# Kernel optimization log

Measured on AMD Instinct MI355X. Metric: run time of the kernel, lower is better.

## Reference

```python
import jax, jax.numpy as jnp
import numpy as np

N = 50000          # nodes
E = 1600000        # edges (avg degree 32)
IN_C, HID_C, OUT_C = 256, 256, 256


def setup_inputs() -> dict:
    key = jax.random.key(0)
    ks = jax.random.split(key, 10)
    x = jax.random.normal(ks[0], (N, IN_C), dtype=jnp.float32)
    edge_index = jax.random.randint(ks[1], (2, E), 0, N, dtype=jnp.int32)
    edge_weight = jax.random.uniform(ks[2], (E,), dtype=jnp.float32)
    W1 = jax.random.normal(ks[3], (IN_C, HID_C), dtype=jnp.float32) / np.float32(np.sqrt(IN_C))
    b1 = jnp.zeros((HID_C,), dtype=jnp.float32)
    W2 = jax.random.normal(ks[4], (HID_C, OUT_C), dtype=jnp.float32) / np.float32(np.sqrt(HID_C))
    b2 = jnp.zeros((OUT_C,), dtype=jnp.float32)
    Wf = jax.random.normal(ks[5], (OUT_C, 1), dtype=jnp.float32) / np.float32(np.sqrt(OUT_C))
    bf = jnp.zeros((1,), dtype=jnp.float32)
    return {"x": x, "edge_index": edge_index, "edge_weight": edge_weight,
            "W1": W1, "b1": b1, "W2": W2, "b2": b2, "Wf": Wf, "bf": bf}


def _gcn_norm(edge_index, edge_weight, num_nodes, dtype):
    # add self loops with weight 1 (PyG gcn_norm default, add_self_loops=True)
    src, dst = edge_index[0], edge_index[1]
    loop = jnp.arange(num_nodes, dtype=edge_index.dtype)
    src_f = jnp.concatenate([src, loop])
    dst_f = jnpp_concat = jnp.concatenate([dst, loop])
    w_f = jnp.concatenate([edge_weight.astype(dtype), jnp.ones((num_nodes,), dtype)])
    # degree over destination nodes (flow source_to_target)
    deg = jax.ops.segment_sum(w_f, dst_f, num_segments=num_nodes)
    dinv = jnp.where(deg > 0, jax.lax.rsqrt(deg), jnp.array(0.0, dtype))
    norm = dinv[src_f] * w_f * dinv[dst_f]   # [E + N]
    return src_f, dst_f, norm


def _gcn_conv(x, src_f, dst_f, norm, W, b):
    h = x @ W                                    # transform first: [N, out]
    msg = h[src_f] * norm[:, None]               # gather + edge-wise scale: [E+N, out]
    agg = jax.ops.segment_sum(msg, dst_f, num_segments=x.shape[0])  # scatter-add
    return agg + b


def reference(x, edge_index, edge_weight, W1, b1, W2, b2, Wf, bf):
    n = x.shape[0]
    src_f, dst_f, norm = _gcn_norm(edge_index, edge_weight, n, x.dtype)
    h = jax.nn.relu(_gcn_conv(x, src_f, dst_f, norm, W1, b1))
    h = jax.nn.relu(_gcn_conv(h, src_f, dst_f, norm, W2, b2))
    out = h @ Wf + bf
    return out
```

## Files before the change

kernel.cpp:

```cpp
#include <hip/hip_runtime.h>
#include <hip/hip_bf16.h>
#include <cstdint>

#define IN_C 256

typedef __attribute__((ext_vector_type(8))) short bf16x8;
typedef __attribute__((ext_vector_type(8))) short s16x8;
typedef __attribute__((ext_vector_type(4))) short s16x4;
typedef __attribute__((ext_vector_type(8))) unsigned short u16x8;
typedef __attribute__((ext_vector_type(4))) float f32x4;

#define FIXED_SCALE 33554432.0f
#define FIXED_INV   (1.0f / 33554432.0f)
#define DEG_MASK    ((1ULL << 40) - 1)

__device__ inline unsigned short f2bf(float f) {
    union { float f; unsigned int u; } v; v.f = f;
    unsigned int r = (v.u + 0x7fffu + ((v.u >> 16) & 1u)) >> 16;
    return (unsigned short)r;
}
__device__ inline float bf2f(unsigned short b) {
    union { unsigned int u; float f; } v; v.u = ((unsigned int)b) << 16;
    return v.f;
}
__device__ inline short2 split1(float f) {
    unsigned short hb = f2bf(f);
    unsigned short lb = f2bf(f - bf2f(hb));
    return make_short2((short)hb, (short)lb);
}

__global__ void deg_count_kernel(const int* __restrict__ ei, const float* __restrict__ w,
                                 unsigned long long* __restrict__ packed,
                                 unsigned short* __restrict__ rank, int E) {
    int e = blockIdx.x * blockDim.x + threadIdx.x;
    if (e >= E) return;
    int dst = ei[E + e];
    unsigned int fx = __float2uint_rn(w[e] * FIXED_SCALE);
    unsigned long long inc = (1ULL << 40) | (unsigned long long)fx;
    unsigned long long old = atomicAdd(&packed[dst], inc);
    rank[e] = (unsigned short)(old >> 40);
}

#define SCAN_B 256
__global__ void scan1_kernel(const unsigned long long* __restrict__ packed,
                             int* __restrict__ rp, int* __restrict__ bsum,
                             float* __restrict__ dinv, int N) {
    __shared__ int s[SCAN_B];
    int tid = threadIdx.x;
    int i = blockIdx.x * SCAN_B + tid;
    int v = 0;
    if (i < N) {
        unsigned long long pk = packed[i];
        v = (int)(pk >> 40);
        float deg = (float)(pk & DEG_MASK) * FIXED_INV;
        dinv[i] = rsqrtf(deg + 1.0f);
    }
    s[tid] = v;
    __syncthreads();
    for (int off = 1; off < SCAN_B; off <<= 1) {
        int t = (tid >= off) ? s[tid - off] : 0;
        __syncthreads();
        s[tid] += t;
        __syncthreads();
    }
    if (i < N) rp[i] = s[tid] - v;
    if (tid == SCAN_B - 1) bsum[blockIdx.x] = s[tid];
}

__global__ void scan2_kernel(int* __restrict__ bsum, int* __restrict__ boff, int nb) {
    __shared__ int s[SCAN_B];
    int tid = threadIdx.x;
    int v = (tid < nb) ? bsum[tid] : 0;
    s[tid] = v;
    __syncthreads();
    for (int off = 1; off < SCAN_B; off <<= 1) {
        int t = (tid >= off) ? s[tid - off] : 0;
        __syncthreads();
        s[tid] += t;
        __syncthreads();
    }
    if (tid < nb) boff[tid] = s[tid] - v;
}

__global__ void scan3_kernel(int* __restrict__ rp, const int* __restrict__ boff,
                             int N, int E) {
    int i = blockIdx.x * blockDim.x + threadIdx.x;
    if (i < N) rp[i] = rp[i] + boff[i >> 8];
    if (i == 0) rp[N] = E;
}

__global__ void fill_kernel(const int* __restrict__ ei, const float* __restrict__ w,
                            const float* __restrict__ dinv,
                            const int* __restrict__ rp,
                            const unsigned short* __restrict__ rank,
                            int2* __restrict__ cv, int E) {
    int e = blockIdx.x * blockDim.x + threadIdx.x;
    if (e >= E) return;
    int src = ei[e];
    int dst = ei[E + e];
    int pos = rp[dst] + (int)rank[e];
    if ((unsigned)pos < (unsigned)E) {
        float v = dinv[src] * w[e] * dinv[dst];
        cv[pos] = make_int2(src, __float_as_int(v));
    }
}

__global__ void prep_kernel(const float* __restrict__ W1, const float* __restrict__ W2,
                            const float* __restrict__ x,
                            unsigned short* __restrict__ w1t_hi, unsigned short* __restrict__ w1t_lo,
                            unsigned short* __restrict__ w2t_hi, unsigned short* __restrict__ w2t_lo,
                            unsigned short* __restrict__ x_hi, unsigned short* __restrict__ x_lo,
                            int nx4) {
    int b = blockIdx.x;
    if (b < 512) {
        const float* W = (b < 256) ? W1 : W2;
        unsigned short* hi = (b < 256) ? w1t_hi : w2t_hi;
        unsigned short* lo = (b < 256) ? w1t_lo : w2t_lo;
        int n = b & 255;
        int k = threadIdx.x;
        float v = W[(size_t)k * 256 + n];
        short2 s = split1(v);
        hi[(size_t)n * 256 + k] = (unsigned short)s.x;
        lo[(size_t)n * 256 + k] = (unsigned short)s.y;
    } else {
        int i = (b - 512) * 256 + threadIdx.x;
        if (i < nx4) {
            float4 v = ((const float4*)x)[i];
            short2 sx = split1(v.x), sy = split1(v.y), sz = split1(v.z), sw = split1(v.w);
            s16x4 hv, lv;
            hv.x = sx.x; hv.y = sy.x; hv.z = sz.x; hv.w = sw.x;
            lv.x = sx.y; lv.y = sy.y; lv.z = sz.y; lv.w = sw.y;
            *(s16x4*)(x_hi + (size_t)i * 4) = hv;
            *(s16x4*)(x_lo + (size_t)i * 4) = lv;
        }
    }
}

template<bool ASPLIT>
__global__ __launch_bounds__(256) void gemm_split_kernel(
    const unsigned short* __restrict__ Ahg,
    const unsigned short* __restrict__ Alg,
    const unsigned short* __restrict__ Bth,
    const unsigned short* __restrict__ Btl,
    unsigned short* __restrict__ C16, int Nrows)
{
    __shared__ __align__(16) short Ah[128 * 64];
    __shared__ __align__(16) short Al[ASPLIT ? 128 * 64 : 8];
    __shared__ __align__(16) short Bh[128 * 64];
    __shared__ __align__(16) short Bl[128 * 64];

    const int t    = threadIdx.x;
    const int lane = t & 63;
    const int w    = t >> 6;
    const int r0   = blockIdx.x * 128;
    const int cb0  = blockIdx.y * 128;
    const int fr   = lane & 15;
    const int fk   = (lane >> 4) * 8;
    const int wm   = w * 32;

    f32x4 acc[2][8] = {};

    for (int k0 = 0; k0 < 256; k0 += 64) {
        __syncthreads();
#pragma unroll
        for (int c = 0; c < 4; ++c) {
            int i = c * 256 + t;
            int row = i >> 3, seg = i & 7;
            size_t g = (size_t)(cb0 + row) * 256 + k0 + seg * 8;
            *(s16x8*)&Bh[row * 64 + seg * 8] = *(const s16x8*)(Bth + g);
            *(s16x8*)&Bl[row * 64 + seg * 8] = *(const s16x8*)(Btl + g);
        }
#pragma unroll
        for (int c = 0; c < 4; ++c) {
            int i = c * 256 + t;
            int row = i >> 3, seg = i & 7;
            int gr = r0 + row; if (gr > Nrows - 1) gr = Nrows - 1;
            size_t g = (size_t)gr * 256 + k0 + seg * 8;
            *(s16x8*)&Ah[row * 64 + seg * 8] = *(const s16x8*)(Ahg + g);
            if constexpr (ASPLIT)
                *(s16x8*)&Al[row * 64 + seg * 8] = *(const s16x8*)(Alg + g);
        }
        __syncthreads();
#pragma unroll
        for (int ks = 0; ks < 2; ++ks) {
            int ko = ks * 32 + fk;
            bf16x8 ah[2], al[2];
#pragma unroll
            for (int mi = 0; mi < 2; ++mi) {
                ah[mi] = *(const bf16x8*)&Ah[(wm + mi * 16 + fr) * 64 + ko];
                if constexpr (ASPLIT)
                    al[mi] = *(const bf16x8*)&Al[(wm + mi * 16 + fr) * 64 + ko];
            }
#pragma unroll
            for (int n = 0; n < 8; ++n) {
                bf16x8 bh = *(const bf16x8*)&Bh[(n * 16 + fr) * 64 + ko];
                bf16x8 bl = *(const bf16x8*)&Bl[(n * 16 + fr) * 64 + ko];
#pragma unroll
                for (int mi = 0; mi < 2; ++mi) {
                    acc[mi][n] = __builtin_amdgcn_mfma_f32_16x16x32_bf16(ah[mi], bh, acc[mi][n], 0, 0, 0);
                    acc[mi][n] = __builtin_amdgcn_mfma_f32_16x16x32_bf16(ah[mi], bl, acc[mi][n], 0, 0, 0);
                    if constexpr (ASPLIT)
                        acc[mi][n] = __builtin_amdgcn_mfma_f32_16x16x32_bf16(al[mi], bh, acc[mi][n], 0, 0, 0);
                }
            }
        }
    }
    const int rb = (lane >> 4) * 4;
#pragma unroll
    for (int mi = 0; mi < 2; ++mi) {
#pragma unroll
        for (int n = 0; n < 8; ++n) {
            int col = cb0 + n * 16 + fr;
#pragma unroll
            for (int r = 0; r < 4; ++r) {
                int row = r0 + wm + mi * 16 + rb + r;
                if (row < Nrows) C16[(size_t)row * 256 + col] = f2bf(acc[mi][n][r]);
            }
        }
    }
}

__device__ inline void fma8(float* acc, u16x8 g, float v) {
#pragma unroll
    for (int c = 0; c < 8; ++c) acc[c] = fmaf(v, bf2f(g[c]), acc[c]);
}

template<int MODE>
__global__ __launch_bounds__(256) void agg_kernel(const unsigned short* __restrict__ h16,
                                                  const int* __restrict__ rp,
                                                  const int2* __restrict__ cv,
                                                  const float* __restrict__ dinv,
                                                  const float* __restrict__ bias,
                                                  unsigned short* __restrict__ out_hi,
                                                  const float* __restrict__ Wf,
                                                  const float* __restrict__ bf,
                                                  float* __restrict__ out,
                                                  int N) {
    int d    = blockIdx.x * 4 + (threadIdx.x >> 6);
    int lane = threadIdx.x & 63;
    if (d >= N) return;
    int half = lane >> 5;
    int co   = (lane & 31) * 8;

    float di = dinv[d];
    float selfm = half ? 0.0f : di * di;
    u16x8 sv = *(const u16x8*)(h16 + (size_t)d * 256 + co);
    float acc[8];
#pragma unroll
    for (int c = 0; c < 8; ++c) acc[c] = selfm * bf2f(sv[c]);

    int s = rp[d], e = rp[d + 1];
    int j = s;
    for (; j + 16 <= e; j += 16) {
        int   ec[8]; float ev[8];
#pragma unroll
        for (int t2 = 0; t2 < 8; ++t2) {
            int2 ca = cv[j + 2 * t2], cb = cv[j + 2 * t2 + 1];
            ec[t2] = half ? cb.x : ca.x;
            ev[t2] = __int_as_float(half ? cb.y : ca.y);
        }
        u16x8 g0 = *(const u16x8*)(h16 + (size_t)ec[0] * 256 + co);
        u16x8 g1 = *(const u16x8*)(h16 + (size_t)ec[1] * 256 + co);
        u16x8 g2 = *(const u16x8*)(h16 + (size_t)ec[2] * 256 + co);
        u16x8 g3 = *(const u16x8*)(h16 + (size_t)ec[3] * 256 + co);
        u16x8 g4 = *(const u16x8*)(h16 + (size_t)ec[4] * 256 + co);
        u16x8 g5 = *(const u16x8*)(h16 + (size_t)ec[5] * 256 + co);
        u16x8 g6 = *(const u16x8*)(h16 + (size_t)ec[6] * 256 + co);
        u16x8 g7 = *(const u16x8*)(h16 + (size_t)ec[7] * 256 + co);
        fma8(acc, g0, ev[0]);
        fma8(acc, g1, ev[1]);
        fma8(acc, g2, ev[2]);
        fma8(acc, g3, ev[3]);
        fma8(acc, g4, ev[4]);
        fma8(acc, g5, ev[5]);
        fma8(acc, g6, ev[6]);
        fma8(acc, g7, ev[7]);
    }
    for (; j + 8 <= e; j += 8) {
        int   ec[4]; float ev[4];
#pragma unroll
        for (int t2 = 0; t2 < 4; ++t2) {
            int2 ca = cv[j + 2 * t2], cb = cv[j + 2 * t2 + 1];
            ec[t2] = half ? cb.x : ca.x;
            ev[t2] = __int_as_float(half ? cb.y : ca.y);
        }
        u16x8 g0 = *(const u16x8*)(h16 + (size_t)ec[0] * 256 + co);
        u16x8 g1 = *(const u16x8*)(h16 + (size_t)ec[1] * 256 + co);
        u16x8 g2 = *(const u16x8*)(h16 + (size_t)ec[2] * 256 + co);
        u16x8 g3 = *(const u16x8*)(h16 + (size_t)ec[3] * 256 + co);
        fma8(acc, g0, ev[0]);
        fma8(acc, g1, ev[1]);
        fma8(acc, g2, ev[2]);
        fma8(acc, g3, ev[3]);
    }
    for (; j + 2 <= e; j += 2) {
        int2 ca = cv[j], cb = cv[j + 1];
        int   ee = half ? cb.x : ca.x;
        float vv = __int_as_float(half ? cb.y : ca.y);
        u16x8 g = *(const u16x8*)(h16 + (size_t)ee * 256 + co);
        fma8(acc, g, vv);
    }
    if (j < e) {
        int2 ca = cv[j];
        int   ee = ca.x;
        float vv = half ? 0.0f : __int_as_float(ca.y);
        u16x8 g = *(const u16x8*)(h16 + (size_t)ee * 256 + co);
        fma8(acc, g, vv);
    }

#pragma unroll
    for (int c = 0; c < 8; ++c) acc[c] += __shfl_xor(acc[c], 32);

    float4 b0 = *(const float4*)(bias + co);
    float4 b1 = *(const float4*)(bias + co + 4);
    acc[0] = fmaxf(acc[0] + b0.x, 0.0f);
    acc[1] = fmaxf(acc[1] + b0.y, 0.0f);
    acc[2] = fmaxf(acc[2] + b0.z, 0.0f);
    acc[3] = fmaxf(acc[3] + b0.w, 0.0f);
    acc[4] = fmaxf(acc[4] + b1.x, 0.0f);
    acc[5] = fmaxf(acc[5] + b1.y, 0.0f);
    acc[6] = fmaxf(acc[6] + b1.z, 0.0f);
    acc[7] = fmaxf(acc[7] + b1.w, 0.0f);

    if constexpr (MODE == 0) {
        if (half == 0) {
            u16x8 hi;
#pragma unroll
            for (int c = 0; c < 8; ++c) hi[c] = f2bf(acc[c]);
            *(u16x8*)(out_hi + (size_t)d * 256 + co) = hi;
        }
    } else {
        float4 wf0 = *(const float4*)(Wf + co);
        float4 wf1 = *(const float4*)(Wf + co + 4);
        float sdot = acc[0] * wf0.x + acc[1] * wf0.y + acc[2] * wf0.z + acc[3] * wf0.w
                   + acc[4] * wf1.x + acc[5] * wf1.y + acc[6] * wf1.z + acc[7] * wf1.w;
        for (int o = 16; o; o >>= 1) sdot += __shfl_down(sdot, o);
        if (lane == 0) out[d] = sdot + bf[0];
    }
}

extern "C" void kernel_launch(void* const* d_in, const int* in_sizes, int n_in,
                              void* d_out, int out_size, void* d_ws, size_t ws_size,
                              hipStream_t stream) {
    const float* x  = (const float*)d_in[0];
    const int*   ei = (const int*)d_in[1];
    const float* w  = (const float*)d_in[2];
    const float* W1 = (const float*)d_in[3];
    const float* b1 = (const float*)d_in[4];
    const float* W2 = (const float*)d_in[5];
    const float* b2 = (const float*)d_in[6];
    const float* Wf = (const float*)d_in[7];
    const float* bf = (const float*)d_in[8];
    float* out = (float*)d_out;

    const int N = in_sizes[0] / IN_C;
    const int E = in_sizes[2];

    auto align256 = [](size_t v) { return (v + 255) & ~(size_t)255; };
    char* p = (char*)d_ws;
    unsigned long long* packed = (unsigned long long*)p; p += align256((size_t)N * 8);
    float* dinv   = (float*)p; p += align256((size_t)N * 4);
    int*   rp     = (int*)p;   p += align256(((size_t)N + 1) * 4);
    int*   bsum   = (int*)p;   p += align256(SCAN_B * 4);
    int*   boff   = (int*)p;   p += align256(SCAN_B * 4);
    unsigned short* rank = (unsigned short*)p; p += align256((size_t)E * 2);
    int2*  cv     = (int2*)p;  p += align256((size_t)E * 8);
    unsigned short* w1t_hi = (unsigned short*)p; p += align256((size_t)256 * 256 * 2);
    unsigned short* w1t_lo = (unsigned short*)p; p += align256((size_t)256 * 256 * 2);
    unsigned short* w2t_hi = (unsigned short*)p; p += align256((size_t)256 * 256 * 2);
    unsigned short* w2t_lo = (unsigned short*)p; p += align256((size_t)256 * 256 * 2);
    unsigned short* hbuf  = (unsigned short*)p; p += align256((size_t)N * 256 * 2);
    unsigned short* xa_hi = (unsigned short*)p; p += align256((size_t)N * 256 * 2);
    unsigned short* xa_lo = (unsigned short*)p; p += align256((size_t)N * 256 * 2);
    (void)ws_size; (void)n_in; (void)out_size;

    const int nb_edges = (E + 255) / 256;
    const int nb_nodes = (N + 255) / 256;
    const int nb_scan  = (N + SCAN_B - 1) / SCAN_B;
    const int nx4      = N * 256 / 4;

    hipMemsetAsync(packed, 0, (size_t)N * 8, stream);

    deg_count_kernel<<<nb_edges, 256, 0, stream>>>(ei, w, packed, rank, E);
    scan1_kernel<<<nb_scan, SCAN_B, 0, stream>>>(packed, rp, bsum, dinv, N);
    scan2_kernel<<<1, SCAN_B, 0, stream>>>(bsum, boff, nb_scan);
    scan3_kernel<<<nb_nodes, 256, 0, stream>>>(rp, boff, N, E);
    fill_kernel<<<nb_edges, 256, 0, stream>>>(ei, w, dinv, rp, rank, cv, E);

    prep_kernel<<<512 + (nx4 + 255) / 256, 256, 0, stream>>>(
        W1, W2, x, w1t_hi, w1t_lo, w2t_hi, w2t_lo, xa_hi, xa_lo, nx4);

    dim3 ggrid((N + 127) / 128, 2);
    const int nb_agg = (N + 3) / 4;

    gemm_split_kernel<true><<<ggrid, 256, 0, stream>>>(xa_hi, xa_lo,
                                                       w1t_hi, w1t_lo, hbuf, N);
    agg_kernel<0><<<nb_agg, 256, 0, stream>>>(hbuf, rp, cv, dinv, b1,
                                              xa_hi, nullptr, nullptr, nullptr, N);
    gemm_split_kernel<false><<<ggrid, 256, 0, stream>>>(xa_hi, nullptr,
                                                        w2t_hi, w2t_lo, hbuf, N);
    agg_kernel<1><<<nb_agg, 256, 0, stream>>>(hbuf, rp, cv, dinv, b2,
                                              nullptr, Wf, bf, out, N);
}
```

Before: 454.9 us.

## Fuse graph-build stages with weight/input prep and GEMM1; drop x low-part split

After: 489.6 us. 1.08x slower.

```diff
diff --git a/kernel.cpp b/kernel.cpp
--- a/kernel.cpp
+++ b/kernel.cpp
@@ -6,7 +6,6 @@
 
 typedef __attribute__((ext_vector_type(8))) short bf16x8;
 typedef __attribute__((ext_vector_type(8))) short s16x8;
-typedef __attribute__((ext_vector_type(4))) short s16x4;
 typedef __attribute__((ext_vector_type(8))) unsigned short u16x8;
 typedef __attribute__((ext_vector_type(4))) float f32x4;
 
@@ -29,16 +28,46 @@
     return make_short2((short)hb, (short)lb);
 }
 
-__global__ void deg_count_kernel(const int* __restrict__ ei, const float* __restrict__ w,
-                                 unsigned long long* __restrict__ packed,
-                                 unsigned short* __restrict__ rank, int E) {
-    int e = blockIdx.x * blockDim.x + threadIdx.x;
-    if (e >= E) return;
-    int dst = ei[E + e];
-    unsigned int fx = __float2uint_rn(w[e] * FIXED_SCALE);
-    unsigned long long inc = (1ULL << 40) | (unsigned long long)fx;
-    unsigned long long old = atomicAdd(&packed[dst], inc);
-    rank[e] = (unsigned short)(old >> 40);
+__global__ void build1_kernel(const int* __restrict__ ei, const float* __restrict__ w,
+                              unsigned long long* __restrict__ packed,
+                              unsigned short* __restrict__ rank, int E, int nbE,
+                              const float* __restrict__ W1, const float* __restrict__ W2,
+                              unsigned short* __restrict__ w1t_hi, unsigned short* __restrict__ w1t_lo,
+                              unsigned short* __restrict__ w2t_hi, unsigned short* __restrict__ w2t_lo,
+                              const float* __restrict__ x, unsigned short* __restrict__ x16,
+                              int nx8) {
+    int b = blockIdx.x;
+    if (b < nbE) {
+        int e = b * 256 + threadIdx.x;
+        if (e < E) {
+            int dst = ei[E + e];
+            unsigned int fx = __float2uint_rn(w[e] * FIXED_SCALE);
+            unsigned long long inc = (1ULL << 40) | (unsigned long long)fx;
+            unsigned long long old = atomicAdd(&packed[dst], inc);
+            rank[e] = (unsigned short)(old >> 40);
+        }
+    } else if (b < nbE + 512) {
+        int bb = b - nbE;
+        const float* W = (bb < 256) ? W1 : W2;
+        unsigned short* hi = (bb < 256) ? w1t_hi : w2t_hi;
+        unsigned short* lo = (bb < 256) ? w1t_lo : w2t_lo;
+        int n = bb & 255;
+        int k = threadIdx.x;
+        float v = W[(size_t)k * 256 + n];
+        short2 s = split1(v);
+        hi[(size_t)n * 256 + k] = (unsigned short)s.x;
+        lo[(size_t)n * 256 + k] = (unsigned short)s.y;
+    } else {
+        int i = (b - nbE - 512) * 256 + threadIdx.x;
+        if (i < nx8) {
+            const float4* xp = (const float4*)x + 2 * (size_t)i;
+            float4 v0 = xp[0], v1 = xp[1];
+            u16x8 o;
+            o[0] = f2bf(v0.x); o[1] = f2bf(v0.y); o[2] = f2bf(v0.z); o[3] = f2bf(v0.w);
+            o[4] = f2bf(v1.x); o[5] = f2bf(v1.y); o[6] = f2bf(v1.z); o[7] = f2bf(v1.w);
+            *(u16x8*)(x16 + (size_t)i * 8) = o;
+        }
+    }
 }
 
 #define SCAN_B 256
@@ -89,71 +118,20 @@
     if (i == 0) rp[N] = E;
 }
 
-__global__ void fill_kernel(const int* __restrict__ ei, const float* __restrict__ w,
-                            const float* __restrict__ dinv,
-                            const int* __restrict__ rp,
-                            const unsigned short* __restrict__ rank,
-                            int2* __restrict__ cv, int E) {
-    int e = blockIdx.x * blockDim.x + threadIdx.x;
-    if (e >= E) return;
-    int src = ei[e];
-    int dst = ei[E + e];
-    int pos = rp[dst] + (int)rank[e];
-    if ((unsigned)pos < (unsigned)E) {
-        float v = dinv[src] * w[e] * dinv[dst];
-        cv[pos] = make_int2(src, __float_as_int(v));
-    }
-}
-
-__global__ void prep_kernel(const float* __restrict__ W1, const float* __restrict__ W2,
-                            const float* __restrict__ x,
-                            unsigned short* __restrict__ w1t_hi, unsigned short* __restrict__ w1t_lo,
-                            unsigned short* __restrict__ w2t_hi, unsigned short* __restrict__ w2t_lo,
-                            unsigned short* __restrict__ x_hi, unsigned short* __restrict__ x_lo,
-                            int nx4) {
-    int b = blockIdx.x;
-    if (b < 512) {
-        const float* W = (b < 256) ? W1 : W2;
-        unsigned short* hi = (b < 256) ? w1t_hi : w2t_hi;
-        unsigned short* lo = (b < 256) ? w1t_lo : w2t_lo;
-        int n = b & 255;
-        int k = threadIdx.x;
-        float v = W[(size_t)k * 256 + n];
-        short2 s = split1(v);
-        hi[(size_t)n * 256 + k] = (unsigned short)s.x;
-        lo[(size_t)n * 256 + k] = (unsigned short)s.y;
-    } else {
-        int i = (b - 512) * 256 + threadIdx.x;
-        if (i < nx4) {
-            float4 v = ((const float4*)x)[i];
-            short2 sx = split1(v.x), sy = split1(v.y), sz = split1(v.z), sw = split1(v.w);
-            s16x4 hv, lv;
-            hv.x = sx.x; hv.y = sy.x; hv.z = sz.x; hv.w = sw.x;
-            lv.x = sx.y; lv.y = sy.y; lv.z = sz.y; lv.w = sw.y;
-            *(s16x4*)(x_hi + (size_t)i * 4) = hv;
-            *(s16x4*)(x_lo + (size_t)i * 4) = lv;
-        }
-    }
-}
-
-template<bool ASPLIT>
-__global__ __launch_bounds__(256) void gemm_split_kernel(
-    const unsigned short* __restrict__ Ahg,
-    const unsigned short* __restrict__ Alg,
-    const unsigned short* __restrict__ Bth,
-    const unsigned short* __restrict__ Btl,
-    unsigned short* __restrict__ C16, int Nrows)
-{
+__device__ inline void gemm_body(const unsigned short* __restrict__ A16,
+                                 const unsigned short* __restrict__ Bth,
+                                 const unsigned short* __restrict__ Btl,
+                                 unsigned short* __restrict__ C16, int Nrows,
+                                 int bx, int by) {
     __shared__ __align__(16) short Ah[128 * 64];
-    __shared__ __align__(16) short Al[ASPLIT ? 128 * 64 : 8];
     __shared__ __align__(16) short Bh[128 * 64];
     __shared__ __align__(16) short Bl[128 * 64];
 
     const int t    = threadIdx.x;
     const int lane = t & 63;
     const int w    = t >> 6;
-    const int r0   = blockIdx.x * 128;
-    const int cb0  = blockIdx.y * 128;
+    const int r0   = bx * 128;
+    const int cb0  = by * 128;
     const int fr   = lane & 15;
     const int fk   = (lane >> 4) * 8;
     const int wm   = w * 32;
@@ -176,21 +154,16 @@
             int row = i >> 3, seg = i & 7;
             int gr = r0 + row; if (gr > Nrows - 1) gr = Nrows - 1;
             size_t g = (size_t)gr * 256 + k0 + seg * 8;
-            *(s16x8*)&Ah[row * 64 + seg * 8] = *(const s16x8*)(Ahg + g);
-            if constexpr (ASPLIT)
-                *(s16x8*)&Al[row * 64 + seg * 8] = *(const s16x8*)(Alg + g);
+            *(s16x8*)&Ah[row * 64 + seg * 8] = *(const s16x8*)(A16 + g);
         }
         __syncthreads();
 #pragma unroll
         for (int ks = 0; ks < 2; ++ks) {
             int ko = ks * 32 + fk;
-            bf16x8 ah[2], al[2];
-#pragma unroll
-            for (int mi = 0; mi < 2; ++mi) {
+            bf16x8 ah[2];
+#pragma unroll
+            for (int mi = 0; mi < 2; ++mi)
                 ah[mi] = *(const bf16x8*)&Ah[(wm + mi * 16 + fr) * 64 + ko];
-                if constexpr (ASPLIT)
-                    al[mi] = *(const bf16x8*)&Al[(wm + mi * 16 + fr) * 64 + ko];
-            }
 #pragma unroll
             for (int n = 0; n < 8; ++n) {
                 bf16x8 bh = *(const bf16x8*)&Bh[(n * 16 + fr) * 64 + ko];
@@ -199,8 +172,6 @@
                 for (int mi = 0; mi < 2; ++mi) {
                     acc[mi][n] = __builtin_amdgcn_mfma_f32_16x16x32_bf16(ah[mi], bh, acc[mi][n], 0, 0, 0);
                     acc[mi][n] = __builtin_amdgcn_mfma_f32_16x16x32_bf16(ah[mi], bl, acc[mi][n], 0, 0, 0);
-                    if constexpr (ASPLIT)
-                        acc[mi][n] = __builtin_amdgcn_mfma_f32_16x16x32_bf16(al[mi], bh, acc[mi][n], 0, 0, 0);
                 }
             }
         }
@@ -218,6 +189,39 @@
             }
         }
     }
+}
+
+__global__ __launch_bounds__(256) void build2_kernel(
+    const int* __restrict__ ei, const float* __restrict__ w,
+    const float* __restrict__ dinv, const int* __restrict__ rp,
+    const unsigned short* __restrict__ rank, int2* __restrict__ cv,
+    int E, int nbE,
+    const unsigned short* __restrict__ A16,
+    const unsigned short* __restrict__ Bth, const unsigned short* __restrict__ Btl,
+    unsigned short* __restrict__ C16, int Nrows) {
+    int b = blockIdx.x;
+    if (b < nbE) {
+        int e = b * 256 + threadIdx.x;
+        if (e < E) {
+            int src = ei[e];
+            int dst = ei[E + e];
+            int pos = rp[dst] + (int)rank[e];
+            if ((unsigned)pos < (unsigned)E) {
+                float v = dinv[src] * w[e] * dinv[dst];
+                cv[pos] = make_int2(src, __float_as_int(v));
+            }
+        }
+    } else {
+        int g = b - nbE;
+        gemm_body(A16, Bth, Btl, C16, Nrows, g >> 1, g & 1);
+    }
+}
+
+__global__ __launch_bounds__(256) void gemm_kernel(
+    const unsigned short* __restrict__ A16,
+    const unsigned short* __restrict__ Bth, const unsigned short* __restrict__ Btl,
+    unsigned short* __restrict__ C16, int Nrows) {
+    gemm_body(A16, Bth, Btl, C16, Nrows, blockIdx.x, blockIdx.y);
 }
 
 __device__ inline void fma8(float* acc, u16x8 g, float v) {
@@ -370,35 +374,36 @@
     unsigned short* w2t_hi = (unsigned short*)p; p += align256((size_t)256 * 256 * 2);
     unsigned short* w2t_lo = (unsigned short*)p; p += align256((size_t)256 * 256 * 2);
     unsigned short* hbuf  = (unsigned short*)p; p += align256((size_t)N * 256 * 2);
-    unsigned short* xa_hi = (unsigned short*)p; p += align256((size_t)N * 256 * 2);
-    unsigned short* xa_lo = (unsigned short*)p; p += align256((size_t)N * 256 * 2);
+    unsigned short* xa16 = (unsigned short*)p; p += align256((size_t)N * 256 * 2);
     (void)ws_size; (void)n_in; (void)out_size;
 
-    const int nb_edges = (E + 255) / 256;
+    const int nbE     = (E + 255) / 256;
     const int nb_nodes = (N + 255) / 256;
     const int nb_scan  = (N + SCAN_B - 1) / SCAN_B;
-    const int nx4      = N * 256 / 4;
+    const int nx8      = N * 256 / 8;
+    const int nb_x     = (nx8 + 255) / 256;
+    const int nb_gemm  = ((N + 127) / 128) * 2;
 
     hipMemsetAsync(packed, 0, (size_t)N * 8, stream);
 
-    deg_count_kernel<<<nb_edges, 256, 0, stream>>>(ei, w, packed, rank, E);
+    build1_kernel<<<nbE + 512 + nb_x, 256, 0, stream>>>(
+        ei, w, packed, rank, E, nbE,
+        W1, W2, w1t_hi, w1t_lo, w2t_hi, w2t_lo, x, xa16, nx8);
+
     scan1_kernel<<<nb_scan, SCAN_B, 0, stream>>>(packed, rp, bsum, dinv, N);
     scan2_kernel<<<1, SCAN_B, 0, stream>>>(bsum, boff, nb_scan);
     scan3_kernel<<<nb_nodes, 256, 0, stream>>>(rp, boff, N, E);
-    fill_kernel<<<nb_edges, 256, 0, stream>>>(ei, w, dinv, rp, rank, cv, E);
-
-    prep_kernel<<<512 + (nx4 + 255) / 256, 256, 0, stream>>>(
-        W1, W2, x, w1t_hi, w1t_lo, w2t_hi, w2t_lo, xa_hi, xa_lo, nx4);
-
+
+    build2_kernel<<<nbE + nb_gemm, 256, 0, stream>>>(
+        ei, w, dinv, rp, rank, cv, E, nbE,
+        xa16, w1t_hi, w1t_lo, hbuf, N);
+
+    const int nb_agg = (N + 3) / 4;
     dim3 ggrid((N + 127) / 128, 2);
-    const int nb_agg = (N + 3) / 4;
-
-    gemm_split_kernel<true><<<ggrid, 256, 0, stream>>>(xa_hi, xa_lo,
-                                                       w1t_hi, w1t_lo, hbuf, N);
+
     agg_kernel<0><<<nb_agg, 256, 0, stream>>>(hbuf, rp, cv, dinv, b1,
-                                              xa_hi, nullptr, nullptr, nullptr, N);
-    gemm_split_kernel<false><<<ggrid, 256, 0, stream>>>(xa_hi, nullptr,
-                                                        w2t_hi, w2t_lo, hbuf, N);
+                                              xa16, nullptr, nullptr, nullptr, N);
+    gemm_kernel<<<ggrid, 256, 0, stream>>>(xa16, w2t_hi, w2t_lo, hbuf, N);
     agg_kernel<1><<<nb_agg, 256, 0, stream>>>(hbuf, rp, cv, dinv, b2,
                                               nullptr, Wf, bf, out, N);
 }
```
